# Kernel tuning notes

Measured on AMD Instinct MI355X. Metric: run time of the kernel, lower is better.

Reference implementation:

```python
import jax, jax.numpy as jnp
import numpy as np

BS, RAL, LAL = 64, 2048, 250
CS, VOC, HFS, EMB = 256, 34, 512, 256


def _lstm_cell(x, h, c, Wih, Whh, bih, bhh):
    # torch.nn.LSTMCell gate order: i, f, g, o
    gates = x @ Wih.T + bih + h @ Whh.T + bhh
    i, f, g, o = jnp.split(gates, 4, axis=-1)
    c_new = jax.nn.sigmoid(f) * c + jax.nn.sigmoid(i) * jnp.tanh(g)
    h_new = jax.nn.sigmoid(o) * jnp.tanh(c_new)
    return h_new, c_new


def setup_inputs() -> dict:
    k0 = jax.random.key(0)
    ks = jax.random.split(k0, 20)
    s = 0.05
    inp = {
        'key': jax.random.normal(ks[0], (BS, RAL, CS), jnp.float32),
        'val': jax.random.normal(ks[1], (BS, RAL, CS), jnp.float32),
        'y': jax.random.randint(ks[2], (BS, LAL), 0, VOC, jnp.int64),
        'mask': jnp.ones((BS, RAL), jnp.float32),
        'emb_table': jax.random.normal(ks[3], (VOC, EMB), jnp.float32) * s,
        'Wih_a': jax.random.normal(ks[4], (4 * HFS, EMB + CS), jnp.float32) * s,
        'Whh_a': jax.random.normal(ks[5], (4 * HFS, HFS), jnp.float32) * s,
        'bih_a': jnp.zeros((4 * HFS,), jnp.float32),
        'bhh_a': jnp.zeros((4 * HFS,), jnp.float32),
        'Wih_b': jax.random.normal(ks[6], (4 * HFS, HFS), jnp.float32) * s,
        'Whh_b': jax.random.normal(ks[7], (4 * HFS, HFS), jnp.float32) * s,
        'bih_b': jnp.zeros((4 * HFS,), jnp.float32),
        'bhh_b': jnp.zeros((4 * HFS,), jnp.float32),
        'Wq': jax.random.normal(ks[8], (CS, HFS), jnp.float32) * s,
        'bq': jnp.zeros((CS,), jnp.float32),
        'Wc': jax.random.normal(ks[9], (VOC, HFS + CS), jnp.float32) * s,
        'bc': jnp.zeros((VOC,), jnp.float32),
    }
    return inp


def reference(key, val, mask, emb_table, Wih_a, Whh_a, bih_a, bhh_a,
              Wih_b, Whh_b, bih_b, bhh_b, Wq, bq, Wc, bc, y):
    bs = key.shape[0]
    emb_seq = emb_table[y]                       # (BS, LAL, EMB)
    emb_seq = jnp.swapaxes(emb_seq, 0, 1)        # (LAL, BS, EMB)
    neg = jnp.asarray(-1e9, key.dtype)
    valid = mask > 0                             # (BS, RAL)

    h_a0 = jnp.zeros((bs, HFS), key.dtype)
    init = (h_a0, h_a0, h_a0, h_a0, jnp.zeros((bs, CS), key.dtype))

    def step(carry, emb_t):
        h_a, c_a, h_b, c_b, context = carry
        lstm_in = jnp.concatenate([emb_t, context], axis=1)      # (BS, EMB+CS)
        h_a, c_a = _lstm_cell(lstm_in, h_a, c_a, Wih_a, Whh_a, bih_a, bhh_a)
        h_b, c_b = _lstm_cell(h_a, h_b, c_b, Wih_b, Whh_b, bih_b, bhh_b)
        query = h_b @ Wq.T + bq                                  # (BS, CS)
        energy = jnp.einsum('brc,bc->br', key, query)            # (BS, RAL)
        energy = jnp.where(valid, energy, neg)
        attention = jax.nn.softmax(energy, axis=-1)
        context = jnp.einsum('br,brc->bc', attention, val)       # (BS, CS)
        y_next = jnp.concatenate([h_b, context], axis=1) @ Wc.T + bc  # (BS, VOC)
        return (h_a, c_a, h_b, c_b, context), y_next

    _, pred = jax.lax.scan(step, init, emb_seq)  # (LAL, BS, VOC)
    return jnp.swapaxes(pred, 0, 1)              # (BS, LAL, VOC)
```

## Files before the change

### kernel.cpp

```cpp
#include <hip/hip_runtime.h>

typedef _Float16 h2 __attribute__((ext_vector_type(2)));
typedef _Float16 h4 __attribute__((ext_vector_type(4)));
typedef _Float16 h8 __attribute__((ext_vector_type(8)));
union H8 { h8 v; h2 p[4]; };

#define AGENT __HIP_MEMORY_SCOPE_AGENT

__device__ __forceinline__ float dot2(h2 a, h2 b, float c) {
#if __has_builtin(__builtin_amdgcn_fdot2)
  return __builtin_amdgcn_fdot2(a, b, c, false);
#else
  return c + (float)a[0]*(float)b[0] + (float)a[1]*(float)b[1];
#endif
}
__device__ __forceinline__ float dot8(h8 x, h8 w, float acc) {
  H8 a, b; a.v = x; b.v = w;
  acc = dot2(a.p[0], b.p[0], acc); acc = dot2(a.p[1], b.p[1], acc);
  acc = dot2(a.p[2], b.p[2], acc); acc = dot2(a.p[3], b.p[3], acc);
  return acc;
}
__device__ __forceinline__ float sigm(float x){ return 1.f/(1.f+__expf(-x)); }

enum : unsigned long long {
  OFF_CA   = 4096ull,
  OFF_CB   = 135168ull,
  OFF_HA   = 266240ull,
  OFF_HB   = 397312ull,
  OFF_CTX  = 528384ull,
  ZERO_W32 = 140288ull,
  OFF_PART = 561152ull,
  OFF_PEMB = 839680ull,
  OFF_BB   = 1118208ull,
  OFF_FLAG = 1126400ull,
  OFF_WA   = 1126656ull,
  OFF_WB   = 4272384ull,
  OFF_WQ   = 8466688ull,
  OFF_WC   = 8728832ull,
  OFF_K16  = 8782080ull,
  OFF_V16  = 75890944ull,
  TOTAL_FULL = 142999808ull
};

#define S3_HBS  0
#define S3_QH   1536
#define S3_PL   2048
#define S3_RED  4096
#define S3_YRED 12288
#define S3_SCAL 13568
#define EX_OFF  132096
#define YS_OFF  134144
#define SMEM_BYTES 135168

struct P {
  const float *key, *val, *mask, *bq, *bc;
  const void* y;
  const _Float16 *k16, *v16;
  float *Pemb, *bb;
  _Float16 *Wa, *Wb, *Wq, *Wc;
  float *ca, *cb, *parts;
  _Float16 *ha, *hb, *ctx;
  unsigned *gctr, *grel, *qctr;
  const int* flag;
  float* out;
};

__device__ __forceinline__ void gsync(unsigned* ctr, unsigned* rel, int e) {
  __syncthreads();
  if (threadIdx.x == 0) {
    __threadfence();
    unsigned a = __hip_atomic_fetch_add(ctr, 1u, __ATOMIC_RELAXED, AGENT);
    if (a == (unsigned)(e*256 - 1)) {
      __hip_atomic_store(rel, (unsigned)e, __ATOMIC_RELEASE, AGENT);
    } else {
      while (__hip_atomic_load(rel, __ATOMIC_RELAXED, AGENT) < (unsigned)e)
        __builtin_amdgcn_s_sleep(2);
    }
    __threadfence();
  }
  __syncthreads();
}

template<int K, bool YS>
__device__ __forceinline__ void lstm_phase(char* sm, int wg, int tid,
    const _Float16* src0, int len0, const _Float16* src1,
    const _Float16* Wcat, const float* accInit,
    const void* yv, int yIs64, int t,
    float* cSt, _Float16* hOut)
{
  constexpr int SK = K/8;
  const int S0 = len0/8;
  h8* xs = (h8*)sm;
  int* ysL = (int*)(sm + YS_OFF);
  if (YS && tid < 64) {
    long idx = (long)tid*250 + t;
    ysL[tid] = yIs64 ? (int)((const long long*)yv)[idx] : ((const int*)yv)[idx];
  }
  for (int i = tid; i < 64*SK; i += 512) {
    int b_ = i / SK, k8 = i % SK;
    const _Float16* s = (k8 < S0) ? (src0 + b_*len0 + k8*8)
                                  : (src1 + b_*512 + (k8 - S0)*8);
    xs[b_*(SK+1) + k8] = *(const h8*)s;
  }
  __syncthreads();
  const int b = tid & 63, r8 = tid >> 6;
  const int jj = r8 & 1, g = r8 >> 1;
  const int n = g*512 + wg*2 + jj;
  float acc = YS ? accInit[ysL[b]*2048 + n] : accInit[n];
  const h8* wrow = (const h8*)(Wcat + (size_t)n*K);
  const h8* xrow = xs + b*(SK+1);
  #pragma unroll 4
  for (int k8 = 0; k8 < SK; ++k8) acc = dot8(xrow[k8], wrow[k8], acc);
  float* ex = (float*)(sm + EX_OFF);
  ex[r8*64 + b] = acc;
  __syncthreads();
  if (tid < 128) {
    int j2 = tid >> 6, b2 = tid & 63;
    float iv = ex[(0+j2)*64+b2], fv = ex[(2+j2)*64+b2];
    float gv = ex[(4+j2)*64+b2], ov = ex[(6+j2)*64+b2];
    int ci = b2*512 + wg*2 + j2;
    float cn = sigm(fv)*cSt[ci] + sigm(iv)*tanhf(gv);
    cSt[ci] = cn;
    hOut[ci] = (_Float16)(sigm(ov)*tanhf(cn));
  }
}

template<bool KV16>
__device__ __forceinline__ void attn(char* sm, const P& p, int wg, int tid, int t, int wrB) {
  const int b = wg >> 2, quarter = wg & 3;
  _Float16* hbs = (_Float16*)(sm + S3_HBS);
  _Float16* qh  = (_Float16*)(sm + S3_QH);
  float* pl   = (float*)(sm + S3_PL);
  float* red  = (float*)(sm + S3_RED);
  float* yred = (float*)(sm + S3_YRED);
  float* scal = (float*)(sm + S3_SCAL);
  hbs[tid] = p.hb[wrB*32768 + b*512 + (tid & 511)];
  __syncthreads();
  if (tid < 256) {
    float a = p.bq[tid];
    const h8* wr = (const h8*)(p.Wq + (size_t)tid*512);
    const h8* hx = (const h8*)hbs;
    #pragma unroll 4
    for (int k = 0; k < 64; ++k) a = dot8(hx[k], wr[k], a);
    qh[tid] = (_Float16)a;
  }
  __syncthreads();
  {
    const int l = tid & 63, wv = tid >> 6, lr = l >> 4, lc = l & 15;
    h2 q2[8]; float qf[16];
    if constexpr (KV16) {
      const h2* qp = (const h2*)qh;
      #pragma unroll
      for (int j = 0; j < 8; ++j) q2[j] = qp[lc*8 + j];
    } else {
      #pragma unroll
      for (int j = 0; j < 16; ++j) qf[j] = (float)qh[lc*16 + j];
    }
    const size_t base = ((size_t)b*2048 + quarter*512 + wv*64 + lr)*256 + lc*16;
    for (int it = 0; it < 16; ++it) {
      int rl = wv*64 + it*4 + lr;
      float e = 0.f;
      if constexpr (KV16) {
        const h8* kp = (const h8*)(p.k16 + base + (size_t)it*4*256);
        H8 a0, a1; a0.v = kp[0]; a1.v = kp[1];
        e = dot2(a0.p[0], q2[0], e); e = dot2(a0.p[1], q2[1], e);
        e = dot2(a0.p[2], q2[2], e); e = dot2(a0.p[3], q2[3], e);
        e = dot2(a1.p[0], q2[4], e); e = dot2(a1.p[1], q2[5], e);
        e = dot2(a1.p[2], q2[6], e); e = dot2(a1.p[3], q2[7], e);
      } else {
        const float4* kp = (const float4*)(p.key + base + (size_t)it*4*256);
        #pragma unroll
        for (int j = 0; j < 4; ++j) {
          float4 kv = kp[j];
          e += kv.x*qf[j*4+0] + kv.y*qf[j*4+1] + kv.z*qf[j*4+2] + kv.w*qf[j*4+3];
        }
      }
      e += __shfl_xor(e, 1); e += __shfl_xor(e, 2);
      e += __shfl_xor(e, 4); e += __shfl_xor(e, 8);
      if (lc == 0) {
        int r = quarter*512 + rl;
        pl[rl] = (p.mask[b*2048 + r] > 0.f) ? e : -1e9f;
      }
    }
  }
  __syncthreads();
  {
    float v = pl[tid], m = v;
    #pragma unroll
    for (int s2 = 32; s2; s2 >>= 1) m = fmaxf(m, __shfl_xor(m, s2));
    if (!(tid & 63)) red[tid >> 6] = m;
    __syncthreads();
    if (!tid) {
      float mm = red[0];
      for (int i = 1; i < 8; ++i) mm = fmaxf(mm, red[i]);
      scal[0] = mm;
    }
    __syncthreads();
    float pe = __expf(v - scal[0]);
    pl[tid] = pe;
    float s = pe;
    #pragma unroll
    for (int s2 = 32; s2; s2 >>= 1) s += __shfl_xor(s, s2);
    if (!(tid & 63)) red[tid >> 6] = s;
    __syncthreads();
    if (!tid) {
      float ss = 0;
      for (int i = 0; i < 8; ++i) ss += red[i];
      scal[1] = ss;
    }
    __syncthreads();
  }
  {
    const int c4 = (tid & 63)*4, rs = tid >> 6;
    float a0 = 0, a1 = 0, a2 = 0, a3 = 0;
    const size_t base = ((size_t)b*2048 + quarter*512 + rs*64)*256 + c4;
    for (int i = 0; i < 64; ++i) {
      float pr = pl[rs*64 + i];
      if constexpr (KV16) {
        h4 v4 = *(const h4*)(p.v16 + base + (size_t)i*256);
        a0 += pr*(float)v4[0]; a1 += pr*(float)v4[1];
        a2 += pr*(float)v4[2]; a3 += pr*(float)v4[3];
      } else {
        float4 v4 = *(const float4*)(p.val + base + (size_t)i*256);
        a0 += pr*v4.x; a1 += pr*v4.y; a2 += pr*v4.z; a3 += pr*v4.w;
      }
    }
    ((float4*)red)[tid] = make_float4(a0, a1, a2, a3);
  }
  __syncthreads();
  if (tid < 256) {
    float s = 0;
    #pragma unroll
    for (int r8 = 0; r8 < 8; ++r8) s += red[r8*256 + tid];
    float* pb = p.parts + (size_t)b*1088 + quarter*272;
    pb[tid] = s;
    if (!tid) { pb[256] = scal[0]; pb[257] = scal[1]; }
  }
  __syncthreads();
  if (!tid) {
    __threadfence();
    __hip_atomic_fetch_add(p.qctr + b, 1u, __ATOMIC_RELAXED, AGENT);
  }
  if (quarter == 0) {
    if (!tid) {
      while (__hip_atomic_load(p.qctr + b, __ATOMIC_RELAXED, AGENT) < 4u*(unsigned)(t+1))
        __builtin_amdgcn_s_sleep(2);
      __threadfence();
    }
    __syncthreads();
    if (tid < 256) {
      const float* pb = p.parts + (size_t)b*1088;
      float m0 = pb[256], s0 = pb[257], m1 = pb[272+256], s1 = pb[272+257];
      float m2 = pb[544+256], s2 = pb[544+257], m3 = pb[816+256], s3 = pb[816+257];
      float M = fmaxf(fmaxf(m0, m1), fmaxf(m2, m3));
      float w0 = __expf(m0-M), w1 = __expf(m1-M), w2 = __expf(m2-M), w3 = __expf(m3-M);
      float S = w0*s0 + w1*s1 + w2*s2 + w3*s3;
      float cv = (w0*pb[tid] + w1*pb[272+tid] + w2*pb[544+tid] + w3*pb[816+tid]) / S;
      hbs[512 + tid] = (_Float16)cv;
      p.ctx[b*256 + tid] = (_Float16)cv;
    }
    __syncthreads();
    {
      int vq = tid >> 3, ks = tid & 7;
      if (vq < 34) {
        float a = 0;
        const h8* wr = (const h8*)(p.Wc + (size_t)vq*768 + ks*96);
        const h8* xx = (const h8*)hbs + ks*12;
        #pragma unroll
        for (int i = 0; i < 12; ++i) a = dot8(xx[i], wr[i], a);
        yred[vq*8 + ks] = a;
      }
    }
    __syncthreads();
    if (tid < 34) {
      float a = p.bc[tid];
      #pragma unroll
      for (int k = 0; k < 8; ++k) a += yred[tid*8 + k];
      p.out[((size_t)b*250 + t)*34 + tid] = a;
    }
  }
}

template<bool KV16>
__global__ __launch_bounds__(512, 2) void speller_main(P p) {
  __shared__ __align__(16) char sm[SMEM_BYTES];
  const int wg = blockIdx.x, tid = threadIdx.x;
  const int y64 = *p.flag;
  int ep = 0;
  for (int t = 0; t < 250; ++t) {
    const int rd = t & 1, wr = 1 - rd;
    lstm_phase<768, true>(sm, wg, tid, p.ctx, 256, p.ha + rd*32768, p.Wa,
                          p.Pemb, p.y, y64, t, p.ca, p.ha + wr*32768);
    gsync(p.gctr, p.grel, ++ep);
    lstm_phase<1024, false>(sm, wg, tid, p.ha + wr*32768, 512, p.hb + rd*32768, p.Wb,
                            p.bb, nullptr, 0, 0, p.cb, p.hb + wr*32768);
    gsync(p.gctr, p.grel, ++ep);
    attn<KV16>(sm, p, wg, tid, t, wr);
    gsync(p.gctr, p.grel, ++ep);
  }
}

__global__ void prep_a(P p, const float* emb, const float* Wih_a, const float* Whh_a,
    const float* bih_a, const float* bhh_a, const float* Wih_b, const float* Whh_b,
    const float* bih_b, const float* bhh_b, const float* Wqf, const float* Wcf,
    unsigned* zb, int* flag)
{
  int id = blockIdx.x*blockDim.x + threadIdx.x;
  int N = gridDim.x*blockDim.x;
  for (int i = id; i < (int)ZERO_W32; i += N) zb[i] = 0u;
  for (int i = id; i < 34*2048; i += N) {
    int v = i >> 11, n = i & 2047;
    float a = bih_a[n] + bhh_a[n];
    const float4* e4 = (const float4*)(emb + v*256);
    const float4* w4 = (const float4*)(Wih_a + (size_t)n*512);
    for (int k = 0; k < 64; ++k) {
      float4 x = e4[k], w = w4[k];
      a += x.x*w.x + x.y*w.y + x.z*w.z + x.w*w.w;
    }
    p.Pemb[i] = a;
  }
  for (int i = id; i < 2048*768; i += N) {
    int n = i / 768, k = i % 768;
    float w = (k < 256) ? Wih_a[(size_t)n*512 + 256 + k] : Whh_a[(size_t)n*512 + k - 256];
    p.Wa[i] = (_Float16)w;
  }
  for (int i = id; i < 2048*1024; i += N) {
    int n = i >> 10, k = i & 1023;
    float w = (k < 512) ? Wih_b[(size_t)n*512 + k] : Whh_b[(size_t)n*512 + k - 512];
    p.Wb[i] = (_Float16)w;
  }
  for (int i = id; i < 256*512; i += N) p.Wq[i] = (_Float16)Wqf[i];
  for (int i = id; i < 34*768; i += N) p.Wc[i] = (_Float16)Wcf[i];
  for (int i = id; i < 2048; i += N) p.bb[i] = bih_b[i] + bhh_b[i];
  if (id == 0) {
    const long long* yl = (const long long*)p.y;
    int ok = 1;
    for (int i = 0; i < 200; ++i) { long long v = yl[i]; if (v < 0 || v >= 34) { ok = 0; break; } }
    *flag = ok;
  }
}

__global__ void prep_kv(const float* key, const float* val, _Float16* k16, _Float16* v16) {
  int id = blockIdx.x*blockDim.x + threadIdx.x;
  int N = gridDim.x*blockDim.x;
  const int PER = 8388608;
  for (int i = id; i < 2*PER; i += N) {
    const float4* src; _Float16* dst; int j;
    if (i < PER) { src = (const float4*)key; dst = k16; j = i; }
    else         { src = (const float4*)val; dst = v16; j = i - PER; }
    float4 x = src[j];
    h4 o; o[0] = (_Float16)x.x; o[1] = (_Float16)x.y; o[2] = (_Float16)x.z; o[3] = (_Float16)x.w;
    *(h4*)(dst + (size_t)j*4) = o;
  }
}

extern "C" void kernel_launch(void* const* d_in, const int* in_sizes, int n_in,
                              void* d_out, int out_size, void* d_ws, size_t ws_size,
                              hipStream_t stream) {
  char* ws = (char*)d_ws;
  P p;
  p.key = (const float*)d_in[0];
  p.val = (const float*)d_in[1];
  p.y   = d_in[2];
  p.mask = (const float*)d_in[3];
  p.bq = (const float*)d_in[14];
  p.bc = (const float*)d_in[16];
  p.gctr = (unsigned*)(ws + 0);
  p.grel = (unsigned*)(ws + 4);
  p.qctr = (unsigned*)(ws + 256);
  p.ca = (float*)(ws + OFF_CA);
  p.cb = (float*)(ws + OFF_CB);
  p.ha = (_Float16*)(ws + OFF_HA);
  p.hb = (_Float16*)(ws + OFF_HB);
  p.ctx = (_Float16*)(ws + OFF_CTX);
  p.parts = (float*)(ws + OFF_PART);
  p.Pemb = (float*)(ws + OFF_PEMB);
  p.bb = (float*)(ws + OFF_BB);
  p.flag = (const int*)(ws + OFF_FLAG);
  p.Wa = (_Float16*)(ws + OFF_WA);
  p.Wb = (_Float16*)(ws + OFF_WB);
  p.Wq = (_Float16*)(ws + OFF_WQ);
  p.Wc = (_Float16*)(ws + OFF_WC);
  p.k16 = (const _Float16*)(ws + OFF_K16);
  p.v16 = (const _Float16*)(ws + OFF_V16);
  p.out = (float*)d_out;

  bool kv16 = ws_size >= (size_t)TOTAL_FULL;

  prep_a<<<dim3(1024), dim3(256), 0, stream>>>(p,
      (const float*)d_in[4], (const float*)d_in[5], (const float*)d_in[6],
      (const float*)d_in[7], (const float*)d_in[8], (const float*)d_in[9],
      (const float*)d_in[10], (const float*)d_in[11], (const float*)d_in[12],
      (const float*)d_in[13], (const float*)d_in[15],
      (unsigned*)ws, (int*)(ws + OFF_FLAG));
  if (kv16) {
    prep_kv<<<dim3(4096), dim3(256), 0, stream>>>(p.key, p.val,
        (_Float16*)(ws + OFF_K16), (_Float16*)(ws + OFF_V16));
    speller_main<true><<<dim3(256), dim3(512), 0, stream>>>(p);
  } else {
    speller_main<false><<<dim3(256), dim3(512), 0, stream>>>(p);
  }
}
```

Baseline: 41.57 ms.

## Double block size to 1024 threads and split LSTM and attention work across them

Raises the persistent speller kernel from 512 to 1024 threads per block. The LSTM dot products are split in half along K, with the two partials and the bias combined in the gate epilogue. Attention is reworked so each thread covers fewer key rows and prefetches key/value vectors into registers before computing, which exposes more memory-level parallelism. In exchange the reductions get larger (32 partial rows instead of 8), register pressure per thread rises under launch_bounds(1024,4), and the softmax pass has to mask out the extra threads.

```diff
diff --git a/kernel.cpp b/kernel.cpp
--- a/kernel.cpp
+++ b/kernel.cpp
@@ -6,6 +6,7 @@
 union H8 { h8 v; h2 p[4]; };
 
 #define AGENT __HIP_MEMORY_SCOPE_AGENT
+#define NT 1024
 
 __device__ __forceinline__ float dot2(h2 a, h2 b, float c) {
 #if __has_builtin(__builtin_amdgcn_fdot2)
@@ -46,11 +47,11 @@
 #define S3_QH   1536
 #define S3_PL   2048
 #define S3_RED  4096
-#define S3_YRED 12288
-#define S3_SCAL 13568
+#define S3_YRED 36864
+#define S3_SCAL 38016
 #define EX_OFF  132096
-#define YS_OFF  134144
-#define SMEM_BYTES 135168
+#define YS_OFF  136192
+#define SMEM_BYTES 136448
 
 struct P {
   const float *key, *val, *mask, *bq, *bc;
@@ -96,28 +97,38 @@
     long idx = (long)tid*250 + t;
     ysL[tid] = yIs64 ? (int)((const long long*)yv)[idx] : ((const int*)yv)[idx];
   }
-  for (int i = tid; i < 64*SK; i += 512) {
+  for (int i = tid; i < 64*SK; i += NT) {
     int b_ = i / SK, k8 = i % SK;
     const _Float16* s = (k8 < S0) ? (src0 + b_*len0 + k8*8)
                                   : (src1 + b_*512 + (k8 - S0)*8);
     xs[b_*(SK+1) + k8] = *(const h8*)s;
   }
   __syncthreads();
-  const int b = tid & 63, r8 = tid >> 6;
-  const int jj = r8 & 1, g = r8 >> 1;
+  const int b = tid & 63, rs = tid >> 6;
+  const int jj = rs & 1, g = (rs >> 1) & 3, s = rs >> 3;
   const int n = g*512 + wg*2 + jj;
-  float acc = YS ? accInit[ysL[b]*2048 + n] : accInit[n];
+  float acc = 0.f;
   const h8* wrow = (const h8*)(Wcat + (size_t)n*K);
   const h8* xrow = xs + b*(SK+1);
-  #pragma unroll 4
-  for (int k8 = 0; k8 < SK; ++k8) acc = dot8(xrow[k8], wrow[k8], acc);
+  #pragma unroll 8
+  for (int m = 0; m < SK/2; ++m) acc = dot8(xrow[2*m+s], wrow[2*m+s], acc);
   float* ex = (float*)(sm + EX_OFF);
-  ex[r8*64 + b] = acc;
+  ex[rs*64 + b] = acc;
   __syncthreads();
   if (tid < 128) {
     int j2 = tid >> 6, b2 = tid & 63;
-    float iv = ex[(0+j2)*64+b2], fv = ex[(2+j2)*64+b2];
-    float gv = ex[(4+j2)*64+b2], ov = ex[(6+j2)*64+b2];
+    int n0 = wg*2 + j2;
+    float i0, i1, i2, i3;
+    if (YS) {
+      const float* pe = accInit + (size_t)ysL[b2]*2048 + n0;
+      i0 = pe[0]; i1 = pe[512]; i2 = pe[1024]; i3 = pe[1536];
+    } else {
+      i0 = accInit[n0]; i1 = accInit[512+n0]; i2 = accInit[1024+n0]; i3 = accInit[1536+n0];
+    }
+    float iv = ex[(0+j2)*64+b2] + ex[(8+0+j2)*64+b2] + i0;
+    float fv = ex[(2+j2)*64+b2] + ex[(8+2+j2)*64+b2] + i1;
+    float gv = ex[(4+j2)*64+b2] + ex[(8+4+j2)*64+b2] + i2;
+    float ov = ex[(6+j2)*64+b2] + ex[(8+6+j2)*64+b2] + i3;
     int ci = b2*512 + wg*2 + j2;
     float cn = sigm(fv)*cSt[ci] + sigm(iv)*tanhf(gv);
     cSt[ci] = cn;
@@ -134,61 +145,84 @@
   float* red  = (float*)(sm + S3_RED);
   float* yred = (float*)(sm + S3_YRED);
   float* scal = (float*)(sm + S3_SCAL);
-  hbs[tid] = p.hb[wrB*32768 + b*512 + (tid & 511)];
+  if (tid < 512) hbs[tid] = p.hb[wrB*32768 + b*512 + tid];
   __syncthreads();
   if (tid < 256) {
     float a = p.bq[tid];
     const h8* wr = (const h8*)(p.Wq + (size_t)tid*512);
     const h8* hx = (const h8*)hbs;
-    #pragma unroll 4
+    #pragma unroll 8
     for (int k = 0; k < 64; ++k) a = dot8(hx[k], wr[k], a);
     qh[tid] = (_Float16)a;
   }
   __syncthreads();
   {
     const int l = tid & 63, wv = tid >> 6, lr = l >> 4, lc = l & 15;
-    h2 q2[8]; float qf[16];
+    const int rbase = quarter*512 + wv*32 + lr;
     if constexpr (KV16) {
+      h2 q2[8];
       const h2* qp = (const h2*)qh;
       #pragma unroll
       for (int j = 0; j < 8; ++j) q2[j] = qp[lc*8 + j];
-    } else {
-      #pragma unroll
-      for (int j = 0; j < 16; ++j) qf[j] = (float)qh[lc*16 + j];
-    }
-    const size_t base = ((size_t)b*2048 + quarter*512 + wv*64 + lr)*256 + lc*16;
-    for (int it = 0; it < 16; ++it) {
-      int rl = wv*64 + it*4 + lr;
-      float e = 0.f;
-      if constexpr (KV16) {
-        const h8* kp = (const h8*)(p.k16 + base + (size_t)it*4*256);
-        H8 a0, a1; a0.v = kp[0]; a1.v = kp[1];
+      const _Float16* kbase = p.k16 + ((size_t)b*2048 + rbase)*256 + lc*16;
+      h8 ka[8], kb[8];
+      #pragma unroll
+      for (int it = 0; it < 8; ++it) {
+        const h8* kp = (const h8*)(kbase + (size_t)it*4*256);
+        ka[it] = kp[0]; kb[it] = kp[1];
+      }
+      #pragma unroll
+      for (int it = 0; it < 8; ++it) {
+        float e = 0.f;
+        H8 a0, a1; a0.v = ka[it]; a1.v = kb[it];
         e = dot2(a0.p[0], q2[0], e); e = dot2(a0.p[1], q2[1], e);
         e = dot2(a0.p[2], q2[2], e); e = dot2(a0.p[3], q2[3], e);
         e = dot2(a1.p[0], q2[4], e); e = dot2(a1.p[1], q2[5], e);
         e = dot2(a1.p[2], q2[6], e); e = dot2(a1.p[3], q2[7], e);
-      } else {
-        const float4* kp = (const float4*)(p.key + base + (size_t)it*4*256);
-        #pragma unroll
-        for (int j = 0; j < 4; ++j) {
-          float4 kv = kp[j];
-          e += kv.x*qf[j*4+0] + kv.y*qf[j*4+1] + kv.z*qf[j*4+2] + kv.w*qf[j*4+3];
-        }
-      }
-      e += __shfl_xor(e, 1); e += __shfl_xor(e, 2);
-      e += __shfl_xor(e, 4); e += __shfl_xor(e, 8);
-      if (lc == 0) {
-        int r = quarter*512 + rl;
-        pl[rl] = (p.mask[b*2048 + r] > 0.f) ? e : -1e9f;
+        e += __shfl_xor(e, 1); e += __shfl_xor(e, 2);
+        e += __shfl_xor(e, 4); e += __shfl_xor(e, 8);
+        if (lc == 0) {
+          int rl = wv*32 + it*4 + lr;
+          pl[rl] = (p.mask[b*2048 + quarter*512 + rl] > 0.f) ? e : -1e9f;
+        }
+      }
+    } else {
+      float qf[16];
+      #pragma unroll
+      for (int j = 0; j < 16; ++j) qf[j] = (float)qh[lc*16 + j];
+      const float* kbase = p.key + ((size_t)b*2048 + rbase)*256 + lc*16;
+      for (int ii = 0; ii < 4; ++ii) {
+        float4 kv[2][4];
+        #pragma unroll
+        for (int jt = 0; jt < 2; ++jt) {
+          const float4* kp = (const float4*)(kbase + (size_t)(ii*2+jt)*4*256);
+          #pragma unroll
+          for (int j = 0; j < 4; ++j) kv[jt][j] = kp[j];
+        }
+        #pragma unroll
+        for (int jt = 0; jt < 2; ++jt) {
+          float e = 0.f;
+          #pragma unroll
+          for (int j = 0; j < 4; ++j)
+            e += kv[jt][j].x*qf[j*4+0] + kv[jt][j].y*qf[j*4+1]
+               + kv[jt][j].z*qf[j*4+2] + kv[jt][j].w*qf[j*4+3];
+          e += __shfl_xor(e, 1); e += __shfl_xor(e, 2);
+          e += __shfl_xor(e, 4); e += __shfl_xor(e, 8);
+          if (lc == 0) {
+            int rl = wv*32 + (ii*2+jt)*4 + lr;
+            pl[rl] = (p.mask[b*2048 + quarter*512 + rl] > 0.f) ? e : -1e9f;
+          }
+        }
       }
     }
   }
   __syncthreads();
   {
-    float v = pl[tid], m = v;
+    float v = (tid < 512) ? pl[tid] : -1e30f;
+    float m = v;
     #pragma unroll
     for (int s2 = 32; s2; s2 >>= 1) m = fmaxf(m, __shfl_xor(m, s2));
-    if (!(tid & 63)) red[tid >> 6] = m;
+    if (tid < 512 && !(tid & 63)) red[tid >> 6] = m;
     __syncthreads();
     if (!tid) {
       float mm = red[0];
@@ -196,12 +230,12 @@
       scal[0] = mm;
     }
     __syncthreads();
-    float pe = __expf(v - scal[0]);
-    pl[tid] = pe;
+    float pe = 0.f;
+    if (tid < 512) { pe = __expf(v - scal[0]); pl[tid] = pe; }
     float s = pe;
     #pragma unroll
     for (int s2 = 32; s2; s2 >>= 1) s += __shfl_xor(s, s2);
-    if (!(tid & 63)) red[tid >> 6] = s;
+    if (tid < 512 && !(tid & 63)) red[tid >> 6] = s;
     __syncthreads();
     if (!tid) {
       float ss = 0;
@@ -211,27 +245,50 @@
     __syncthreads();
   }
   {
-    const int c4 = (tid & 63)*4, rs = tid >> 6;
-    float a0 = 0, a1 = 0, a2 = 0, a3 = 0;
-    const size_t base = ((size_t)b*2048 + quarter*512 + rs*64)*256 + c4;
-    for (int i = 0; i < 64; ++i) {
-      float pr = pl[rs*64 + i];
-      if constexpr (KV16) {
-        h4 v4 = *(const h4*)(p.v16 + base + (size_t)i*256);
-        a0 += pr*(float)v4[0]; a1 += pr*(float)v4[1];
-        a2 += pr*(float)v4[2]; a3 += pr*(float)v4[3];
-      } else {
-        float4 v4 = *(const float4*)(p.val + base + (size_t)i*256);
-        a0 += pr*v4.x; a1 += pr*v4.y; a2 += pr*v4.z; a3 += pr*v4.w;
-      }
-    }
-    ((float4*)red)[tid] = make_float4(a0, a1, a2, a3);
+    const int l32 = tid & 31, rs32 = tid >> 5;
+    float a[8] = {0,0,0,0,0,0,0,0};
+    if constexpr (KV16) {
+      const _Float16* vbase = p.v16 + ((size_t)b*2048 + quarter*512 + rs32*16)*256 + l32*8;
+      #pragma unroll
+      for (int ii = 0; ii < 2; ++ii) {
+        h8 vv[8];
+        #pragma unroll
+        for (int j = 0; j < 8; ++j) vv[j] = *(const h8*)(vbase + (size_t)(ii*8+j)*256);
+        #pragma unroll
+        for (int j = 0; j < 8; ++j) {
+          float pr = pl[rs32*16 + ii*8 + j];
+          #pragma unroll
+          for (int c = 0; c < 8; ++c) a[c] += pr * (float)vv[j][c];
+        }
+      }
+    } else {
+      const float* vbase = p.val + ((size_t)b*2048 + quarter*512 + rs32*16)*256 + l32*8;
+      for (int ii = 0; ii < 4; ++ii) {
+        float4 v4[4][2];
+        #pragma unroll
+        for (int j = 0; j < 4; ++j) {
+          const float4* vp = (const float4*)(vbase + (size_t)(ii*4+j)*256);
+          v4[j][0] = vp[0]; v4[j][1] = vp[1];
+        }
+        #pragma unroll
+        for (int j = 0; j < 4; ++j) {
+          float pr = pl[rs32*16 + ii*4 + j];
+          a[0] += pr*v4[j][0].x; a[1] += pr*v4[j][0].y;
+          a[2] += pr*v4[j][0].z; a[3] += pr*v4[j][0].w;
+          a[4] += pr*v4[j][1].x; a[5] += pr*v4[j][1].y;
+          a[6] += pr*v4[j][1].z; a[7] += pr*v4[j][1].w;
+        }
+      }
+    }
+    float* rd = red + rs32*256 + l32*8;
+    ((float4*)rd)[0] = make_float4(a[0], a[1], a[2], a[3]);
+    ((float4*)rd)[1] = make_float4(a[4], a[5], a[6], a[7]);
   }
   __syncthreads();
   if (tid < 256) {
     float s = 0;
     #pragma unroll
-    for (int r8 = 0; r8 < 8; ++r8) s += red[r8*256 + tid];
+    for (int r = 0; r < 32; ++r) s += red[r*256 + tid];
     float* pb = p.parts + (size_t)b*1088 + quarter*272;
     pb[tid] = s;
     if (!tid) { pb[256] = scal[0]; pb[257] = scal[1]; }
@@ -282,7 +339,7 @@
 }
 
 template<bool KV16>
-__global__ __launch_bounds__(512, 2) void speller_main(P p) {
+__global__ __launch_bounds__(NT, 4) void speller_main(P p) {
   __shared__ __align__(16) char sm[SMEM_BYTES];
   const int wg = blockIdx.x, tid = threadIdx.x;
   const int y64 = *p.flag;
@@ -396,8 +453,8 @@
   if (kv16) {
     prep_kv<<<dim3(4096), dim3(256), 0, stream>>>(p.key, p.val,
         (_Float16*)(ws + OFF_K16), (_Float16*)(ws + OFF_V16));
-    speller_main<true><<<dim3(256), dim3(512), 0, stream>>>(p);
+    speller_main<true><<<dim3(256), dim3(NT), 0, stream>>>(p);
   } else {
-    speller_main<false><<<dim3(256), dim3(512), 0, stream>>>(p);
-  }
-}
+    speller_main<false><<<dim3(256), dim3(NT), 0, stream>>>(p);
+  }
+}
```

Result: faster. 39.78 ms (-4.3%).
